# Optimization experiments

Hardware: AMD Instinct MI355X
Metric: run time of the kernel (lower is better)

The kernel has to match this reference:

```python
import jax, jax.numpy as jnp
import numpy as np

N = 50000      # nodes
E = 800000     # edges
IN_DIM = 128
HID = 16       # per-head hidden dim (layer1)
HEADS = 8
OUT_DIM = 32   # layer2 output dim (1 head)
NEG_SLOPE = 0.2  # GAT-paper LeakyReLU slope


def _gat_layer(x, W, a_src, a_dst, src, dst, num_nodes):
    """One multi-head GAT layer.
    x: [N, Fin]; W: [Fin, H*D]; a_src/a_dst: [H, D]; src/dst: [E].
    Returns [N, H, D].
    """
    H, D = a_src.shape
    z = (x @ W).reshape(num_nodes, H, D)            # [N, H, D]
    # edge attention logits: attn_fc([z_src || z_dst]) split into two dots
    e_s = jnp.einsum('nhd,hd->nh', z, a_src)        # [N, H]
    e_d = jnp.einsum('nhd,hd->nh', z, a_dst)        # [N, H]
    e = e_s[src] + e_d[dst]                          # [E, H]
    e = jnp.where(e >= 0, e, NEG_SLOPE * e)          # leaky_relu
    # softmax over incoming edges of each destination node
    m = jax.ops.segment_max(e, dst, num_segments=num_nodes)   # [N, H]
    ex = jnp.exp(e - m[dst])                                   # [E, H]
    s = jax.ops.segment_sum(ex, dst, num_segments=num_nodes)  # [N, H]
    alpha = ex / s[dst]                                        # [E, H]
    msg = alpha[:, :, None] * z[src]                            # [E, H, D]
    return jax.ops.segment_sum(msg, dst, num_segments=num_nodes)  # [N, H, D]


def setup_inputs() -> dict:
    key = jax.random.key(0)
    ks = jax.random.split(key, 9)
    h = jax.random.normal(ks[0], (N, IN_DIM), dtype=jnp.float32)
    src = jax.random.randint(ks[1], (E,), 0, N, dtype=jnp.int32)
    dst = jax.random.randint(ks[2], (E,), 0, N, dtype=jnp.int32)
    sc1 = 1.0 / np.sqrt(IN_DIM)
    W1 = jax.random.normal(ks[3], (IN_DIM, HEADS * HID), dtype=jnp.float32) * sc1
    a1_src = jax.random.normal(ks[4], (HEADS, HID), dtype=jnp.float32) * 0.1
    a1_dst = jax.random.normal(ks[5], (HEADS, HID), dtype=jnp.float32) * 0.1
    sc2 = 1.0 / np.sqrt(HEADS * HID)
    W2 = jax.random.normal(ks[6], (HEADS * HID, OUT_DIM), dtype=jnp.float32) * sc2
    a2_src = jax.random.normal(ks[7], (1, OUT_DIM), dtype=jnp.float32) * 0.1
    a2_dst = jax.random.normal(ks[8], (1, OUT_DIM), dtype=jnp.float32) * 0.1
    return {"h": h, "W1": W1, "a1_src": a1_src, "a1_dst": a1_dst,
            "W2": W2, "a2_src": a2_src, "a2_dst": a2_dst,
            "src": src, "dst": dst}


def reference(h, W1, a1_src, a1_dst, W2, a2_src, a2_dst, src, dst):
    # layer1: multi-head, concat heads -> [N, HEADS*HID]
    h1 = _gat_layer(h, W1, a1_src, a1_dst, src, dst, N).reshape(N, HEADS * HID)
    h1 = jax.nn.elu(h1)
    # layer2: single head -> [N, OUT_DIM]
    out = _gat_layer(h1, W2, a2_src, a2_dst, src, dst, N).reshape(N, OUT_DIM)
    return out
```

## Files before the change

kernel.cpp:

```cpp
#include <hip/hip_runtime.h>
#include <hip/hip_fp16.h>
#include <math.h>

#define NN 50000
#define EE 800000
#define FIN 128
#define F1  128
#define NH  8
#define DH  16
#define F2  32
#define SLOPE 0.2f
#define LOG2E 1.44269504f

#define EB 4096
#define NBLK ((EE + EB - 1) / EB)
#define BK  391
#define SEGCAP 4096
#define PREPB 80
#define GEMM1B ((NN + 63) / 64)
#define ATT1B  (((NN + 127) / 128) * 8)
#define GEMM2B ((NN + 63) / 64)

typedef _Float16 f16x8 __attribute__((ext_vector_type(8)));
typedef float    f32x4 __attribute__((ext_vector_type(4)));

__global__ __launch_bounds__(256) void k1_hist_prep(const int* __restrict__ dst,
        const float* __restrict__ W1, const float* __restrict__ W2,
        __half* __restrict__ wt1, __half* __restrict__ wt2, int* __restrict__ hist) {
    int tid = threadIdx.x;
    if (blockIdx.x < NBLK) {
        __shared__ int lc[BK];
        for (int i = tid; i < BK; i += 256) lc[i] = 0;
        __syncthreads();
        int base = blockIdx.x * EB;
        int end = base + EB; if (end > EE) end = EE;
        for (int i = base + tid; i < end; i += 256)
            atomicAdd(&lc[dst[i] >> 7], 1);
        __syncthreads();
        for (int i = tid; i < BK; i += 256)
            if (lc[i]) atomicAdd(&hist[i], lc[i]);
    } else {
        int gidx = (blockIdx.x - NBLK) * 256 + tid;
        if (gidx < FIN * F1) {
            int n = gidx >> 7, k = gidx & 127;
            wt1[gidx] = __float2half(W1[k * F1 + n]);
        } else {
            int t2 = gidx - FIN * F1;
            if (t2 < F2 * FIN) {
                int n = t2 >> 7, k = t2 & 127;
                wt2[t2] = __float2half(W2[k * F2 + n]);
            }
        }
    }
}

extern __shared__ char smem_k2[];
__global__ __launch_bounds__(256) void k2_split_gemm1(const int* __restrict__ src,
        const int* __restrict__ dst, const int* __restrict__ hist, int* __restrict__ cursor,
        unsigned int* __restrict__ sorted,
        const float* __restrict__ h, const __half* __restrict__ wt1,
        const float* __restrict__ a1s, const float* __restrict__ a1d,
        __half* __restrict__ z1s, float* __restrict__ es1x, float* __restrict__ ed1x) {
    int tid = threadIdx.x;
    if (blockIdx.x < NBLK) {
        unsigned int*   recs = (unsigned int*)smem_k2;
        unsigned short* rbk  = (unsigned short*)(smem_k2 + 16384);
        int* lc    = (int*)(smem_k2 + 24576);
        int* lofs  = (int*)(smem_k2 + 26624);
        int* lcur  = (int*)(smem_k2 + 28672);
        int* delta = (int*)(smem_k2 + 30720);
        int* bscan = (int*)(smem_k2 + 32768);
        int* sh    = (int*)(smem_k2 + 34816);
        for (int i = tid; i < 512; i += 256) lc[i] = 0;
        __syncthreads();
        int base = blockIdx.x * EB;
        int cnt = EE - base; if (cnt > EB) cnt = EB;
        unsigned int myrec[16];
        #pragma unroll
        for (int k = 0; k < 16; ++k) {
            int i = base + tid + k * 256;
            myrec[k] = 0xFFFFFFFFu;
            if (i - base < cnt) {
                unsigned int d = (unsigned int)dst[i];
                myrec[k] = (d << 16) | (unsigned int)src[i];
                atomicAdd(&lc[d >> 7], 1);
            }
        }
        __syncthreads();
        int a0 = lc[2 * tid], a1 = lc[2 * tid + 1];
        int tsum = a0 + a1;
        sh[tid] = tsum;
        __syncthreads();
        for (int off = 1; off < 256; off <<= 1) {
            int t = (tid >= off) ? sh[tid - off] : 0;
            __syncthreads(); sh[tid] += t; __syncthreads();
        }
        int ex = sh[tid] - tsum;
        lofs[2 * tid] = ex;
        lofs[2 * tid + 1] = ex + a0;
        __syncthreads();
        int h0 = hist[2 * tid], h1 = hist[2 * tid + 1];
        int hsum = h0 + h1;
        sh[tid] = hsum;
        __syncthreads();
        for (int off = 1; off < 256; off <<= 1) {
            int t = (tid >= off) ? sh[tid - off] : 0;
            __syncthreads(); sh[tid] += t; __syncthreads();
        }
        int hex = sh[tid] - hsum;
        bscan[2 * tid] = hex;
        bscan[2 * tid + 1] = hex + h0;
        __syncthreads();
        for (int b = tid; b < BK; b += 256) {
            int c = lc[b];
            lcur[b] = lofs[b];
            if (c) {
                int g = atomicAdd(&cursor[b], c);
                delta[b] = bscan[b] + g - lofs[b];
            }
        }
        __syncthreads();
        #pragma unroll
        for (int k = 0; k < 16; ++k) {
            if (myrec[k] != 0xFFFFFFFFu) {
                int b = (int)(myrec[k] >> 23);
                int pos = atomicAdd(&lcur[b], 1);
                recs[pos] = myrec[k];
                rbk[pos] = (unsigned short)b;
            }
        }
        __syncthreads();
        for (int s = tid; s < cnt; s += 256)
            sorted[s + delta[rbk[s]]] = recs[s];
    } else {
        __half* hs  = (__half*)smem_k2;
        __half* wls = (__half*)(smem_k2 + 17408);
        for (int c = tid; c < 2048; c += 256) {
            int row = c >> 4, ch = c & 15;
            *(float4*)&wls[row * 136 + ch * 8] = *(const float4*)&wt1[row * 128 + ch * 8];
        }
        int rowBase = (blockIdx.x - NBLK) * 64;
        for (int idx4 = tid; idx4 < 64 * 32; idx4 += 256) {
            int r = idx4 >> 5, cc = (idx4 & 31) * 4;
            int n = rowBase + r;
            float4 v = (n < NN) ? *(const float4*)&h[(size_t)n * FIN + cc] : make_float4(0, 0, 0, 0);
            union { __half2 h2[2]; int2 i; } u;
            u.h2[0] = __floats2half2_rn(v.x, v.y);
            u.h2[1] = __floats2half2_rn(v.z, v.w);
            *(int2*)&hs[r * 136 + cc] = u.i;
        }
        __syncthreads();
        int l = tid & 63, w = tid >> 6;
        int q = l >> 4, cl = l & 15;
        int m0 = w * 16;
        float as[8], ad[8];
        #pragma unroll
        for (int t = 0; t < 8; ++t) { as[t] = a1s[t * DH + cl]; ad[t] = a1d[t * DH + cl]; }
        f32x4 acc[8];
        #pragma unroll
        for (int t = 0; t < 8; ++t) acc[t] = (f32x4){0.f, 0.f, 0.f, 0.f};
        const __half* ap = &hs[(m0 + cl) * 136 + q * 8];
        const __half* bp = &wls[cl * 136 + q * 8];
        #pragma unroll
        for (int k0 = 0; k0 < 128; k0 += 32) {
            f16x8 af = *(const f16x8*)(ap + k0);
            #pragma unroll
            for (int t = 0; t < 8; ++t) {
                f16x8 bf = *(const f16x8*)(bp + t * 16 * 136 + k0);
                acc[t] = __builtin_amdgcn_mfma_f32_16x16x32_f16(af, bf, acc[t], 0, 0, 0);
            }
        }
        #pragma unroll
        for (int t = 0; t < 8; ++t) {
            #pragma unroll
            for (int reg = 0; reg < 4; ++reg) {
                int row = rowBase + m0 + q * 4 + reg;
                float z = acc[t][reg];
                float s = z * as[t], d = z * ad[t];
                s += __shfl_xor(s, 1, 64); d += __shfl_xor(d, 1, 64);
                s += __shfl_xor(s, 2, 64); d += __shfl_xor(d, 2, 64);
                s += __shfl_xor(s, 4, 64); d += __shfl_xor(d, 4, 64);
                s += __shfl_xor(s, 8, 64); d += __shfl_xor(d, 8, 64);
                if (row < NN) {
                    z1s[(size_t)t * (NN * 16) + (size_t)row * 16 + cl] = __float2half(z);
                    if (cl == 0) {
                        es1x[row * NH + t] = s * LOG2E;
                        ed1x[row * NH + t] = d * LOG2E;
                    }
                }
            }
        }
    }
}

__global__ __launch_bounds__(256) void csrbuild_kernel(const int* __restrict__ hist,
        const unsigned int* __restrict__ sorted, unsigned short* __restrict__ csr,
        unsigned char* __restrict__ dstl,
        const float* __restrict__ es1x, const float* __restrict__ ed1x,
        float* __restrict__ w1p, int* __restrict__ row_ptr) {
    __shared__ unsigned int recs[SEGCAP];
    __shared__ unsigned short csr_sh[SEGCAP];
    __shared__ unsigned char dst_sh[SEGCAP];
    __shared__ float ed_sh[128 * NH];
    __shared__ int ncnt[128], ncur[128];
    __shared__ int sh[256];
    __shared__ int bscan[512];
    int b = blockIdx.x;
    int tid = threadIdx.x;
    int h0 = hist[2 * tid], h1 = hist[2 * tid + 1];
    int hsum = h0 + h1;
    sh[tid] = hsum;
    if (tid < 128) ncnt[tid] = 0;
    for (int idx = tid; idx < 128 * NH; idx += 256) {
        int node = b * 128 + (idx >> 3);
        ed_sh[idx] = (node < NN) ? ed1x[node * NH + (idx & 7)] : 0.f;
    }
    __syncthreads();
    for (int off = 1; off < 256; off <<= 1) {
        int t = (tid >= off) ? sh[tid - off] : 0;
        __syncthreads(); sh[tid] += t; __syncthreads();
    }
    int hex = sh[tid] - hsum;
    bscan[2 * tid] = hex;
    bscan[2 * tid + 1] = hex + h0;
    __syncthreads();
    int s0 = bscan[b], s1 = bscan[b + 1];
    int cnt = s1 - s0; if (cnt > SEGCAP) cnt = SEGCAP;
    for (int i = tid; i < cnt; i += 256) {
        unsigned int r = sorted[s0 + i];
        recs[i] = r;
        atomicAdd(&ncnt[(r >> 16) & 127], 1);
    }
    __syncthreads();
    int v = (tid < 128) ? ncnt[tid] : 0;
    sh[tid] = v;
    __syncthreads();
    for (int off = 1; off < 256; off <<= 1) {
        int t = (tid >= off) ? sh[tid - off] : 0;
        __syncthreads(); sh[tid] += t; __syncthreads();
    }
    int ex = sh[tid] - v;
    if (tid < 128) {
        ncur[tid] = ex;
        int node = b * 128 + tid;
        if (node < NN) row_ptr[node] = s0 + ex;
    }
    if (b == BK - 1 && tid == 0) row_ptr[NN] = EE;
    __syncthreads();
    for (int i = tid; i < cnt; i += 256) {
        unsigned int r = recs[i];
        int local = (r >> 16) & 127;
        int p = atomicAdd(&ncur[local], 1);
        csr_sh[p] = (unsigned short)(r & 0xFFFFu);
        dst_sh[p] = (unsigned char)local;
    }
    __syncthreads();
    for (int i = tid; i < cnt; i += 256) {
        unsigned short sv = csr_sh[i];
        unsigned char lv = dst_sh[i];
        csr[s0 + i] = sv;
        dstl[s0 + i] = lv;
        float4 ea = *(const float4*)&es1x[(size_t)sv * NH];
        float4 eb = *(const float4*)&es1x[(size_t)sv * NH + 4];
        float es8[8] = {ea.x, ea.y, ea.z, ea.w, eb.x, eb.y, eb.z, eb.w};
        const float* edp = &ed_sh[(int)lv * NH];
        #pragma unroll
        for (int hh = 0; hh < 8; ++hh) {
            float e = es8[hh] + edp[hh];
            e = e >= 0.f ? e : SLOPE * e;
            w1p[(size_t)hh * EE + s0 + i] = exp2f(e);
        }
    }
}

__global__ __launch_bounds__(256) void attn1_slice_kernel(const int* __restrict__ row_ptr,
        const unsigned short* __restrict__ csr, const __half* __restrict__ z1s,
        const float* __restrict__ w1p, __half* __restrict__ h1s) {
    int hl = blockIdx.x & 7;
    int n = (blockIdx.x >> 3) * 128 + (threadIdx.x >> 1);
    if (n >= NN) return;
    int j = threadIdx.x & 1;
    const __half* zp = z1s + (size_t)hl * (NN * 16) + j * 8;
    const float* wp = w1p + (size_t)hl * EE;
    int b0 = row_ptr[n];
    int cnt = row_ptr[n + 1] - b0;
    float acc[8] = {0.f, 0.f, 0.f, 0.f, 0.f, 0.f, 0.f, 0.f};
    float ws = 0.f;
    int i = 0;
    for (; i + 4 <= cnt; i += 4) {
        int s0 = csr[b0 + i], s1 = csr[b0 + i + 1], s2 = csr[b0 + i + 2], s3 = csr[b0 + i + 3];
        float w0 = wp[b0 + i], w1 = wp[b0 + i + 1], w2 = wp[b0 + i + 2], w3 = wp[b0 + i + 3];
        union { float4 f; __half2 h2[4]; } u0, u1, u2, u3;
        u0.f = *(const float4*)&zp[(size_t)s0 * 16];
        u1.f = *(const float4*)&zp[(size_t)s1 * 16];
        u2.f = *(const float4*)&zp[(size_t)s2 * 16];
        u3.f = *(const float4*)&zp[(size_t)s3 * 16];
        ws += (w0 + w1) + (w2 + w3);
        #pragma unroll
        for (int t = 0; t < 4; ++t) {
            float2 v0 = __half22float2(u0.h2[t]);
            float2 v1 = __half22float2(u1.h2[t]);
            float2 v2 = __half22float2(u2.h2[t]);
            float2 v3 = __half22float2(u3.h2[t]);
            acc[2*t]   = fmaf(w0, v0.x, fmaf(w1, v1.x, fmaf(w2, v2.x, fmaf(w3, v3.x, acc[2*t]))));
            acc[2*t+1] = fmaf(w0, v0.y, fmaf(w1, v1.y, fmaf(w2, v2.y, fmaf(w3, v3.y, acc[2*t+1]))));
        }
    }
    for (; i < cnt; ++i) {
        int s = csr[b0 + i];
        float wv = wp[b0 + i];
        ws += wv;
        union { float4 f; __half2 h2[4]; } u;
        u.f = *(const float4*)&zp[(size_t)s * 16];
        #pragma unroll
        for (int t = 0; t < 4; ++t) {
            float2 v = __half22float2(u.h2[t]);
            acc[2*t]   = fmaf(wv, v.x, acc[2*t]);
            acc[2*t+1] = fmaf(wv, v.y, acc[2*t+1]);
        }
    }
    float rs = ws > 0.f ? 1.0f / ws : 0.f;
    union { float4 f; __half2 h2[4]; } p;
    #pragma unroll
    for (int t = 0; t < 4; ++t) {
        float x0 = acc[2*t] * rs, x1 = acc[2*t+1] * rs;
        x0 = x0 > 0.f ? x0 : __expf(x0) - 1.0f;
        x1 = x1 > 0.f ? x1 : __expf(x1) - 1.0f;
        p.h2[t] = __floats2half2_rn(x0, x1);
    }
    *(float4*)&h1s[(size_t)hl * (NN * 16) + (size_t)n * 16 + j * 8] = p.f;
}

__global__ __launch_bounds__(256) void gemm2_kernel(const __half* __restrict__ h1s,
        const __half* __restrict__ wt2, const float* __restrict__ a2s, const float* __restrict__ a2d,
        __half* __restrict__ z2h, float* __restrict__ es2x, float* __restrict__ ed2x) {
    __shared__ alignas(16) __half hs[64 * 136];
    __shared__ alignas(16) __half wls[32 * 136];
    int tid = threadIdx.x;
    for (int c = tid; c < 512; c += 256) {
        int row = c >> 4, ch = c & 15;
        *(float4*)&wls[row * 136 + ch * 8] = *(const float4*)&wt2[row * 128 + ch * 8];
    }
    int rowBase = blockIdx.x * 64;
    for (int idx = tid; idx < 1024; idx += 256) {
        int j2 = idx & 1, nl = (idx >> 1) & 63, pl = idx >> 7;
        int n = rowBase + nl;
        float4 v = (n < NN) ? *(const float4*)&h1s[(size_t)pl * (NN * 16) + (size_t)n * 16 + j2 * 8]
                            : make_float4(0, 0, 0, 0);
        *(float4*)&hs[nl * 136 + pl * 16 + j2 * 8] = v;
    }
    __syncthreads();
    int l = tid & 63, w = tid >> 6;
    int q = l >> 4, cl = l & 15;
    int m0 = w * 16;
    float as0 = a2s[cl], as1 = a2s[16 + cl];
    float ad0 = a2d[cl], ad1 = a2d[16 + cl];
    f32x4 acc2[2];
    acc2[0] = (f32x4){0.f, 0.f, 0.f, 0.f};
    acc2[1] = (f32x4){0.f, 0.f, 0.f, 0.f};
    const __half* ap = &hs[(m0 + cl) * 136 + q * 8];
    const __half* bp = &wls[cl * 136 + q * 8];
    #pragma unroll
    for (int k0 = 0; k0 < 128; k0 += 32) {
        f16x8 af = *(const f16x8*)(ap + k0);
        #pragma unroll
        for (int t = 0; t < 2; ++t) {
            f16x8 bf = *(const f16x8*)(bp + t * 16 * 136 + k0);
            acc2[t] = __builtin_amdgcn_mfma_f32_16x16x32_f16(af, bf, acc2[t], 0, 0, 0);
        }
    }
    #pragma unroll
    for (int reg = 0; reg < 4; ++reg) {
        int row = rowBase + m0 + q * 4 + reg;
        float s = acc2[0][reg] * as0 + acc2[1][reg] * as1;
        float d = acc2[0][reg] * ad0 + acc2[1][reg] * ad1;
        s += __shfl_xor(s, 1, 64); d += __shfl_xor(d, 1, 64);
        s += __shfl_xor(s, 2, 64); d += __shfl_xor(d, 2, 64);
        s += __shfl_xor(s, 4, 64); d += __shfl_xor(d, 4, 64);
        s += __shfl_xor(s, 8, 64); d += __shfl_xor(d, 8, 64);
        if (row < NN) {
            z2h[(size_t)row * F2 + cl]      = __float2half(acc2[0][reg]);
            z2h[(size_t)row * F2 + 16 + cl] = __float2half(acc2[1][reg]);
            if (cl == 0) {
                es2x[row] = s * LOG2E;
                ed2x[row] = d * LOG2E;
            }
        }
    }
}

__global__ __launch_bounds__(256) void w2_kernel(const int* __restrict__ row_ptr,
        const unsigned short* __restrict__ csr, const unsigned char* __restrict__ dstl,
        const float* __restrict__ es2x, const float* __restrict__ ed2x,
        float* __restrict__ w2p) {
    int b = blockIdx.x;
    int s0 = row_ptr[b * 128];
    int nend = (b + 1) * 128; if (nend > NN) nend = NN;
    int s1 = row_ptr[nend];
    for (int i = s0 + threadIdx.x; i < s1; i += 256) {
        int s = csr[i];
        int n = b * 128 + (int)dstl[i];
        float e = es2x[s] + ed2x[n];
        e = e >= 0.f ? e : SLOPE * e;
        w2p[i] = exp2f(e);
    }
}

__global__ __launch_bounds__(256) void attn2_kernel(const int* __restrict__ row_ptr,
        const unsigned short* __restrict__ csr, const __half* __restrict__ z2h,
        const float* __restrict__ w2p, float* __restrict__ out) {
    int gt = blockIdx.x * 256 + threadIdx.x;
    int n = gt >> 3;
    int j = gt & 7;
    if (n >= NN) return;
    int b0 = row_ptr[n];
    int cnt = row_ptr[n + 1] - b0;
    float acc[4] = {0.f, 0.f, 0.f, 0.f};
    float ws = 0.f;
    int i = 0;
    for (; i + 4 <= cnt; i += 4) {
        int s0 = csr[b0 + i], s1 = csr[b0 + i + 1], s2 = csr[b0 + i + 2], s3 = csr[b0 + i + 3];
        float w0 = w2p[b0 + i], w1 = w2p[b0 + i + 1], w2 = w2p[b0 + i + 2], w3 = w2p[b0 + i + 3];
        union { float2 f; __half2 h2[2]; } u0, u1, u2, u3;
        u0.f = *(const float2*)&z2h[(size_t)s0 * F2 + j * 4];
        u1.f = *(const float2*)&z2h[(size_t)s1 * F2 + j * 4];
        u2.f = *(const float2*)&z2h[(size_t)s2 * F2 + j * 4];
        u3.f = *(const float2*)&z2h[(size_t)s3 * F2 + j * 4];
        ws += (w0 + w1) + (w2 + w3);
        #pragma unroll
        for (int t = 0; t < 2; ++t) {
            float2 v0 = __half22float2(u0.h2[t]);
            float2 v1 = __half22float2(u1.h2[t]);
            float2 v2 = __half22float2(u2.h2[t]);
            float2 v3 = __half22float2(u3.h2[t]);
            acc[2*t]   = fmaf(w0, v0.x, fmaf(w1, v1.x, fmaf(w2, v2.x, fmaf(w3, v3.x, acc[2*t]))));
            acc[2*t+1] = fmaf(w0, v0.y, fmaf(w1, v1.y, fmaf(w2, v2.y, fmaf(w3, v3.y, acc[2*t+1]))));
        }
    }
    for (; i < cnt; ++i) {
        int s = csr[b0 + i];
        float wv = w2p[b0 + i];
        ws += wv;
        union { float2 f; __half2 h2[2]; } u;
        u.f = *(const float2*)&z2h[(size_t)s * F2 + j * 4];
        #pragma unroll
        for (int t = 0; t < 2; ++t) {
            float2 v = __half22float2(u.h2[t]);
            acc[2*t]   = fmaf(wv, v.x, acc[2*t]);
            acc[2*t+1] = fmaf(wv, v.y, acc[2*t+1]);
        }
    }
    float rs = ws > 0.f ? 1.0f / ws : 0.f;
    *(float4*)&out[(size_t)n * F2 + j * 4] =
        make_float4(acc[0]*rs, acc[1]*rs, acc[2]*rs, acc[3]*rs);
}

extern "C" void kernel_launch(void* const* d_in, const int* in_sizes, int n_in,
                              void* d_out, int out_size, void* d_ws, size_t ws_size,
                              hipStream_t stream) {
    const float* h   = (const float*)d_in[0];
    const float* W1  = (const float*)d_in[1];
    const float* a1s = (const float*)d_in[2];
    const float* a1d = (const float*)d_in[3];
    const float* W2  = (const float*)d_in[4];
    const float* a2s = (const float*)d_in[5];
    const float* a2d = (const float*)d_in[6];
    const int*   src = (const int*)d_in[7];
    const int*   dst = (const int*)d_in[8];
    float* out = (float*)d_out;

    int* ip      = (int*)d_ws;
    int* hist    = ip;
    int* cursor  = hist + 512;
    int* row_ptr = cursor + 512;
    unsigned int* sorted = (unsigned int*)(row_ptr + NN + 8);
    unsigned short* csr16 = (unsigned short*)(sorted + EE);
    unsigned char* dstl = (unsigned char*)(csr16 + EE);
    float* es1x = (float*)(dstl + EE);
    float* ed1x = es1x + (size_t)NN * NH;
    float* es2x = ed1x + (size_t)NN * NH;
    float* ed2x = es2x + NN;
    __half* z1s = (__half*)(ed2x + NN);
    __half* z2h = z1s + (size_t)NN * F1;
    __half* wt1 = z2h + (size_t)NN * F2;
    __half* wt2 = wt1 + FIN * F1;
    __half* h1s = wt2 + F2 * FIN;
    float* w1p  = (float*)(h1s + (size_t)NN * F1);
    float* w2p  = (float*)sorted;

    hipMemsetAsync(hist, 0, 1024 * sizeof(int), stream);

    k1_hist_prep<<<NBLK + PREPB, 256, 0, stream>>>(dst, W1, W2, wt1, wt2, hist);
    k2_split_gemm1<<<NBLK + GEMM1B, 256, 52224, stream>>>(src, dst, hist, cursor, sorted,
                                                          h, wt1, a1s, a1d, z1s, es1x, ed1x);
    csrbuild_kernel<<<BK, 256, 0, stream>>>(hist, sorted, csr16, dstl, es1x, ed1x, w1p, row_ptr);
    attn1_slice_kernel<<<ATT1B, 256, 0, stream>>>(row_ptr, csr16, z1s, w1p, h1s);
    gemm2_kernel<<<GEMM2B, 256, 0, stream>>>(h1s, wt2, a2s, a2d, z2h, es2x, ed2x);
    w2_kernel<<<BK, 256, 0, stream>>>(row_ptr, csr16, dstl, es2x, ed2x, w2p);
    attn2_kernel<<<(NN * 8 + 255) / 256, 256, 0, stream>>>(row_ptr, csr16, z2h, w2p, out);
}
```

Baseline: 212.1 us.

## Fuse layer-2 edge weights into attn2, vectorise attn1 loads, shrink blocks

Removes the separate w2_kernel and its dstl byte array. attn2 now recomputes the leaky-relu/exp2 edge weight on the fly from es2x/ed2x, which saves one kernel launch and an edge-sized write and read. attn1 first handles a short unaligned prefix, then loads csr indices and weights as ushort4/float4 and prefetches the next group one step ahead. Blocks drop to 128 threads for attn1 and attn2, and the histogram uses smaller edge chunks. The cost is more exp2 work in attn2, since each weight is recomputed by all 8 lanes of a node, plus gathers of es2x by source index.

```diff
diff --git a/kernel.cpp b/kernel.cpp
--- a/kernel.cpp
+++ b/kernel.cpp
@@ -14,11 +14,13 @@
 
 #define EB 4096
 #define NBLK ((EE + EB - 1) / EB)
+#define HB 2048
+#define NHBLK ((EE + HB - 1) / HB)
 #define BK  391
 #define SEGCAP 4096
 #define PREPB 80
 #define GEMM1B ((NN + 63) / 64)
-#define ATT1B  (((NN + 127) / 128) * 8)
+#define ATT1B  (((NN + 63) / 64) * 8)
 #define GEMM2B ((NN + 63) / 64)
 
 typedef _Float16 f16x8 __attribute__((ext_vector_type(8)));
@@ -28,19 +30,19 @@
         const float* __restrict__ W1, const float* __restrict__ W2,
         __half* __restrict__ wt1, __half* __restrict__ wt2, int* __restrict__ hist) {
     int tid = threadIdx.x;
-    if (blockIdx.x < NBLK) {
+    if (blockIdx.x < NHBLK) {
         __shared__ int lc[BK];
         for (int i = tid; i < BK; i += 256) lc[i] = 0;
         __syncthreads();
-        int base = blockIdx.x * EB;
-        int end = base + EB; if (end > EE) end = EE;
+        int base = blockIdx.x * HB;
+        int end = base + HB; if (end > EE) end = EE;
         for (int i = base + tid; i < end; i += 256)
             atomicAdd(&lc[dst[i] >> 7], 1);
         __syncthreads();
         for (int i = tid; i < BK; i += 256)
             if (lc[i]) atomicAdd(&hist[i], lc[i]);
     } else {
-        int gidx = (blockIdx.x - NBLK) * 256 + tid;
+        int gidx = (blockIdx.x - NHBLK) * 256 + tid;
         if (gidx < FIN * F1) {
             int n = gidx >> 7, k = gidx & 127;
             wt1[gidx] = __float2half(W1[k * F1 + n]);
@@ -195,7 +197,6 @@
 
 __global__ __launch_bounds__(256) void csrbuild_kernel(const int* __restrict__ hist,
         const unsigned int* __restrict__ sorted, unsigned short* __restrict__ csr,
-        unsigned char* __restrict__ dstl,
         const float* __restrict__ es1x, const float* __restrict__ ed1x,
         float* __restrict__ w1p, int* __restrict__ row_ptr) {
     __shared__ unsigned int recs[SEGCAP];
@@ -259,7 +260,6 @@
         unsigned short sv = csr_sh[i];
         unsigned char lv = dst_sh[i];
         csr[s0 + i] = sv;
-        dstl[s0 + i] = lv;
         float4 ea = *(const float4*)&es1x[(size_t)sv * NH];
         float4 eb = *(const float4*)&es1x[(size_t)sv * NH + 4];
         float es8[8] = {ea.x, ea.y, ea.z, ea.w, eb.x, eb.y, eb.z, eb.w};
@@ -273,11 +273,11 @@
     }
 }
 
-__global__ __launch_bounds__(256) void attn1_slice_kernel(const int* __restrict__ row_ptr,
+__global__ __launch_bounds__(128, 8) void attn1_slice_kernel(const int* __restrict__ row_ptr,
         const unsigned short* __restrict__ csr, const __half* __restrict__ z1s,
         const float* __restrict__ w1p, __half* __restrict__ h1s) {
     int hl = blockIdx.x & 7;
-    int n = (blockIdx.x >> 3) * 128 + (threadIdx.x >> 1);
+    int n = (blockIdx.x >> 3) * 64 + (threadIdx.x >> 1);
     if (n >= NN) return;
     int j = threadIdx.x & 1;
     const __half* zp = z1s + (size_t)hl * (NN * 16) + j * 8;
@@ -287,24 +287,63 @@
     float acc[8] = {0.f, 0.f, 0.f, 0.f, 0.f, 0.f, 0.f, 0.f};
     float ws = 0.f;
     int i = 0;
-    for (; i + 4 <= cnt; i += 4) {
-        int s0 = csr[b0 + i], s1 = csr[b0 + i + 1], s2 = csr[b0 + i + 2], s3 = csr[b0 + i + 3];
-        float w0 = wp[b0 + i], w1 = wp[b0 + i + 1], w2 = wp[b0 + i + 2], w3 = wp[b0 + i + 3];
-        union { float4 f; __half2 h2[4]; } u0, u1, u2, u3;
-        u0.f = *(const float4*)&zp[(size_t)s0 * 16];
-        u1.f = *(const float4*)&zp[(size_t)s1 * 16];
-        u2.f = *(const float4*)&zp[(size_t)s2 * 16];
-        u3.f = *(const float4*)&zp[(size_t)s3 * 16];
-        ws += (w0 + w1) + (w2 + w3);
+    int pre = (4 - (b0 & 3)) & 3; if (pre > cnt) pre = cnt;
+    for (; i < pre; ++i) {
+        int s = csr[b0 + i];
+        float wv = wp[b0 + i];
+        ws += wv;
+        union { float4 f; __half2 h2[4]; } u;
+        u.f = *(const float4*)&zp[(size_t)s * 16];
         #pragma unroll
         for (int t = 0; t < 4; ++t) {
-            float2 v0 = __half22float2(u0.h2[t]);
-            float2 v1 = __half22float2(u1.h2[t]);
-            float2 v2 = __half22float2(u2.h2[t]);
-            float2 v3 = __half22float2(u3.h2[t]);
-            acc[2*t]   = fmaf(w0, v0.x, fmaf(w1, v1.x, fmaf(w2, v2.x, fmaf(w3, v3.x, acc[2*t]))));
-            acc[2*t+1] = fmaf(w0, v0.y, fmaf(w1, v1.y, fmaf(w2, v2.y, fmaf(w3, v3.y, acc[2*t+1]))));
-        }
+            float2 v = __half22float2(u.h2[t]);
+            acc[2*t]   = fmaf(wv, v.x, acc[2*t]);
+            acc[2*t+1] = fmaf(wv, v.y, acc[2*t+1]);
+        }
+    }
+    int nb = (cnt - i) >> 2;
+    if (nb > 0) {
+        int e = b0 + i;
+        ushort4 c4 = *(const ushort4*)&csr[e];
+        float4  w4 = *(const float4*)&wp[e];
+        for (int k = 1; k < nb; ++k) {
+            ushort4 c4n = *(const ushort4*)&csr[e + 4];
+            float4  w4n = *(const float4*)&wp[e + 4];
+            union { float4 f; __half2 h2[4]; } u0, u1, u2, u3;
+            u0.f = *(const float4*)&zp[(size_t)c4.x * 16];
+            u1.f = *(const float4*)&zp[(size_t)c4.y * 16];
+            u2.f = *(const float4*)&zp[(size_t)c4.z * 16];
+            u3.f = *(const float4*)&zp[(size_t)c4.w * 16];
+            ws += (w4.x + w4.y) + (w4.z + w4.w);
+            #pragma unroll
+            for (int t = 0; t < 4; ++t) {
+                float2 v0 = __half22float2(u0.h2[t]);
+                float2 v1 = __half22float2(u1.h2[t]);
+                float2 v2 = __half22float2(u2.h2[t]);
+                float2 v3 = __half22float2(u3.h2[t]);
+                acc[2*t]   = fmaf(w4.x, v0.x, fmaf(w4.y, v1.x, fmaf(w4.z, v2.x, fmaf(w4.w, v3.x, acc[2*t]))));
+                acc[2*t+1] = fmaf(w4.x, v0.y, fmaf(w4.y, v1.y, fmaf(w4.z, v2.y, fmaf(w4.w, v3.y, acc[2*t+1]))));
+            }
+            c4 = c4n; w4 = w4n; e += 4;
+        }
+        {
+            union { float4 f; __half2 h2[4]; } u0, u1, u2, u3;
+            u0.f = *(const float4*)&zp[(size_t)c4.x * 16];
+            u1.f = *(const float4*)&zp[(size_t)c4.y * 16];
+            u2.f = *(const float4*)&zp[(size_t)c4.z * 16];
+            u3.f = *(const float4*)&zp[(size_t)c4.w * 16];
+            ws += (w4.x + w4.y) + (w4.z + w4.w);
+            #pragma unroll
+            for (int t = 0; t < 4; ++t) {
+                float2 v0 = __half22float2(u0.h2[t]);
+                float2 v1 = __half22float2(u1.h2[t]);
+                float2 v2 = __half22float2(u2.h2[t]);
+                float2 v3 = __half22float2(u3.h2[t]);
+                acc[2*t]   = fmaf(w4.x, v0.x, fmaf(w4.y, v1.x, fmaf(w4.z, v2.x, fmaf(w4.w, v3.x, acc[2*t]))));
+                acc[2*t+1] = fmaf(w4.x, v0.y, fmaf(w4.y, v1.y, fmaf(w4.z, v2.y, fmaf(w4.w, v3.y, acc[2*t+1]))));
+            }
+        }
+        i += nb << 2;
     }
     for (; i < cnt; ++i) {
         int s = csr[b0 + i];
@@ -389,43 +428,35 @@
     }
 }
 
-__global__ __launch_bounds__(256) void w2_kernel(const int* __restrict__ row_ptr,
-        const unsigned short* __restrict__ csr, const unsigned char* __restrict__ dstl,
-        const float* __restrict__ es2x, const float* __restrict__ ed2x,
-        float* __restrict__ w2p) {
-    int b = blockIdx.x;
-    int s0 = row_ptr[b * 128];
-    int nend = (b + 1) * 128; if (nend > NN) nend = NN;
-    int s1 = row_ptr[nend];
-    for (int i = s0 + threadIdx.x; i < s1; i += 256) {
-        int s = csr[i];
-        int n = b * 128 + (int)dstl[i];
-        float e = es2x[s] + ed2x[n];
-        e = e >= 0.f ? e : SLOPE * e;
-        w2p[i] = exp2f(e);
-    }
-}
-
-__global__ __launch_bounds__(256) void attn2_kernel(const int* __restrict__ row_ptr,
+__global__ __launch_bounds__(128) void attn2_kernel(const int* __restrict__ row_ptr,
         const unsigned short* __restrict__ csr, const __half* __restrict__ z2h,
-        const float* __restrict__ w2p, float* __restrict__ out) {
-    int gt = blockIdx.x * 256 + threadIdx.x;
+        const float* __restrict__ es, const float* __restrict__ ed,
+        float* __restrict__ out) {
+    int gt = blockIdx.x * 128 + threadIdx.x;
     int n = gt >> 3;
     int j = gt & 7;
     if (n >= NN) return;
     int b0 = row_ptr[n];
     int cnt = row_ptr[n + 1] - b0;
+    float edn = ed[n];
     float acc[4] = {0.f, 0.f, 0.f, 0.f};
     float ws = 0.f;
     int i = 0;
     for (; i + 4 <= cnt; i += 4) {
         int s0 = csr[b0 + i], s1 = csr[b0 + i + 1], s2 = csr[b0 + i + 2], s3 = csr[b0 + i + 3];
-        float w0 = w2p[b0 + i], w1 = w2p[b0 + i + 1], w2 = w2p[b0 + i + 2], w3 = w2p[b0 + i + 3];
+        float e0 = es[s0] + edn;
+        float e1 = es[s1] + edn;
+        float e2 = es[s2] + edn;
+        float e3 = es[s3] + edn;
         union { float2 f; __half2 h2[2]; } u0, u1, u2, u3;
         u0.f = *(const float2*)&z2h[(size_t)s0 * F2 + j * 4];
         u1.f = *(const float2*)&z2h[(size_t)s1 * F2 + j * 4];
         u2.f = *(const float2*)&z2h[(size_t)s2 * F2 + j * 4];
         u3.f = *(const float2*)&z2h[(size_t)s3 * F2 + j * 4];
+        float w0 = exp2f(e0 >= 0.f ? e0 : SLOPE * e0);
+        float w1 = exp2f(e1 >= 0.f ? e1 : SLOPE * e1);
+        float w2 = exp2f(e2 >= 0.f ? e2 : SLOPE * e2);
+        float w3 = exp2f(e3 >= 0.f ? e3 : SLOPE * e3);
         ws += (w0 + w1) + (w2 + w3);
         #pragma unroll
         for (int t = 0; t < 2; ++t) {
@@ -439,7 +470,8 @@
     }
     for (; i < cnt; ++i) {
         int s = csr[b0 + i];
-        float wv = w2p[b0 + i];
+        float e = es[s] + edn;
+        float wv = exp2f(e >= 0.f ? e : SLOPE * e);
         ws += wv;
         union { float2 f; __half2 h2[2]; } u;
         u.f = *(const float2*)&z2h[(size_t)s * F2 + j * 4];
@@ -475,8 +507,7 @@
     int* row_ptr = cursor + 512;
     unsigned int* sorted = (unsigned int*)(row_ptr + NN + 8);
     unsigned short* csr16 = (unsigned short*)(sorted + EE);
-    unsigned char* dstl = (unsigned char*)(csr16 + EE);
-    float* es1x = (float*)(dstl + EE);
+    float* es1x = (float*)(csr16 + EE);
     float* ed1x = es1x + (size_t)NN * NH;
     float* es2x = ed1x + (size_t)NN * NH;
     float* ed2x = es2x + NN;
@@ -486,16 +517,14 @@
     __half* wt2 = wt1 + FIN * F1;
     __half* h1s = wt2 + F2 * FIN;
     float* w1p  = (float*)(h1s + (size_t)NN * F1);
-    float* w2p  = (float*)sorted;
 
     hipMemsetAsync(hist, 0, 1024 * sizeof(int), stream);
 
-    k1_hist_prep<<<NBLK + PREPB, 256, 0, stream>>>(dst, W1, W2, wt1, wt2, hist);
+    k1_hist_prep<<<NHBLK + PREPB, 256, 0, stream>>>(dst, W1, W2, wt1, wt2, hist);
     k2_split_gemm1<<<NBLK + GEMM1B, 256, 52224, stream>>>(src, dst, hist, cursor, sorted,
                                                           h, wt1, a1s, a1d, z1s, es1x, ed1x);
-    csrbuild_kernel<<<BK, 256, 0, stream>>>(hist, sorted, csr16, dstl, es1x, ed1x, w1p, row_ptr);
-    attn1_slice_kernel<<<ATT1B, 256, 0, stream>>>(row_ptr, csr16, z1s, w1p, h1s);
+    csrbuild_kernel<<<BK, 256, 0, stream>>>(hist, sorted, csr16, es1x, ed1x, w1p, row_ptr);
+    attn1_slice_kernel<<<ATT1B, 128, 0, stream>>>(row_ptr, csr16, z1s, w1p, h1s);
     gemm2_kernel<<<GEMM2B, 256, 0, stream>>>(h1s, wt2, a2s, a2d, z2h, es2x, ed2x);
-    w2_kernel<<<BK, 256, 0, stream>>>(row_ptr, csr16, dstl, es2x, ed2x, w2p);
-    attn2_kernel<<<(NN * 8 + 255) / 256, 256, 0, stream>>>(row_ptr, csr16, z2h, w2p, out);
-}
+    attn2_kernel<<<(NN * 8 + 127) / 128, 128, 0, stream>>>(row_ptr, csr16, z2h, es2x, ed2x, out);
+}
```

After: 211.7 us. About the same (-0.2%).
